# Kernel tuning notes

Hardware: AMD Instinct MI355X
Metric: run time of the kernel (lower is better)

The kernel has to match this reference:

```python
import jax, jax.numpy as jnp
import numpy as np

N_NODES = 100_000
N_EDGES = 600_000
D = 128  # in_channels


def setup_inputs() -> dict:
    key = jax.random.key(0)
    k1, k2, k3, k4, k5 = jax.random.split(key, 5)
    node_embs_src = jax.random.normal(k1, (N_NODES, D), dtype=jnp.float32)
    node_embs_dst = jax.random.normal(k2, (N_NODES, D), dtype=jnp.float32)
    edge_index = jax.random.randint(k3, (2, N_EDGES), 0, N_NODES, dtype=jnp.int64)
    # MLP params: Linear(2D -> D), Linear(D -> 1); scaled like default torch init
    W1 = jax.random.normal(k4, (2 * D, D), dtype=jnp.float32) / np.sqrt(2 * D)
    b1 = jnp.zeros((D,), dtype=jnp.float32)
    W2 = jax.random.normal(k5, (D, 1), dtype=jnp.float32) / np.sqrt(D)
    b2 = jnp.zeros((1,), dtype=jnp.float32)
    return {
        "node_embs_src": node_embs_src,
        "node_embs_dst": node_embs_dst,
        "edge_index": edge_index,
        "W1": W1,
        "b1": b1,
        "W2": W2,
        "b2": b2,
    }


def reference(node_embs_src, node_embs_dst, edge_index, W1, b1, W2, b2):
    # Gather per-edge source / destination embeddings: [E, D] each
    src = node_embs_src[edge_index[0]]
    dst = node_embs_dst[edge_index[1]]
    # concat([src, dst]) @ W1 == src @ W1[:D] + dst @ W1[D:]  (avoids materializing [E, 2D])
    h = jnp.dot(src, W1[:D]) + jnp.dot(dst, W1[D:]) + b1  # [E, D]
    h = jax.nn.relu(h)
    logits = jnp.dot(h, W2) + b2  # [E, 1]
    return jax.nn.sigmoid(logits)
```

## Files before the change

### kernel.cpp

```cpp
#include <hip/hip_runtime.h>
#include <stdint.h>

typedef __attribute__((ext_vector_type(8))) short short8;
typedef __attribute__((ext_vector_type(8))) signed char schar8;
typedef __attribute__((ext_vector_type(4))) float f32x4;

__device__ __forceinline__ unsigned short f2bf(float f) {
  union { float f; uint32_t u; } v; v.f = f;
  uint32_t u = v.u;
  uint32_t r = (u + 0x7FFFu + ((u >> 16) & 1u)) >> 16;
  return (unsigned short)r;
}
__device__ __forceinline__ float bf2f(unsigned short h) {
  union { uint32_t u; float f; } v; v.u = ((uint32_t)h) << 16; return v.f;
}

#define NBM 64
__global__ __launch_bounds__(256, 4)
void node_phase_q8(const float* __restrict__ src_emb,
                   const float* __restrict__ dst_emb,
                   const float* __restrict__ W1,
                   const float* __restrict__ b1,
                   int8_t* __restrict__ Q,
                   float* __restrict__ SC,
                   int Nn, int ntiles) {
  __shared__ __align__(16) char Als[NBM * 256];
  __shared__ __align__(16) float pam[NBM][4];

  const int tbl = blockIdx.y;
  const float* emb = tbl ? dst_emb : src_emb;
  const float* Wt  = W1 + (size_t)tbl * 128 * 128;
  int8_t* Qt  = Q  + (size_t)tbl * Nn * 128;
  float*  SCt = SC + (size_t)tbl * Nn;

  const int tid  = threadIdx.x;
  const int lane = tid & 63;
  const int w    = tid >> 6;
  const int l15  = lane & 15;
  const int lk8  = (lane >> 4) * 8;

  short8 bfrag[4][2];
#pragma unroll
  for (int s = 0; s < 4; ++s) {
#pragma unroll
    for (int nf = 0; nf < 2; ++nf) {
      const int col = w * 32 + 2 * l15 + nf;
      short8 t;
#pragma unroll
      for (int j = 0; j < 8; ++j) {
        const int k = s * 32 + lk8 + j;
        t[j] = (short)f2bf(Wt[k * 128 + col]);
      }
      bfrag[s][nf] = t;
    }
  }
  const int colb = w * 32 + 2 * l15;
  const float bias0 = tbl ? 0.f : b1[colb];
  const float bias1 = tbl ? 0.f : b1[colb + 1];

  const int q = tid & 15, r0 = tid >> 4;
  const int swz = (l15 & 7) << 4;
  const int gx = gridDim.x;

  float4 p0[4], p1[4];
#pragma unroll
  for (int i = 0; i < 4; ++i) {
    const int node = blockIdx.x * NBM + i * 16 + r0;
    if (node < Nn) {
      const float* base = emb + (size_t)node * 128 + q * 8;
      p0[i] = *(const float4*)base;
      p1[i] = *(const float4*)(base + 4);
    }
  }

  for (int t = blockIdx.x; t < ntiles; t += gx) {
    const int t0 = t * NBM;

#pragma unroll
    for (int i = 0; i < 4; ++i) {
      const int row = i * 16 + r0;
      short8 hv;
      hv[0] = (short)f2bf(p0[i].x); hv[1] = (short)f2bf(p0[i].y);
      hv[2] = (short)f2bf(p0[i].z); hv[3] = (short)f2bf(p0[i].w);
      hv[4] = (short)f2bf(p1[i].x); hv[5] = (short)f2bf(p1[i].y);
      hv[6] = (short)f2bf(p1[i].z); hv[7] = (short)f2bf(p1[i].w);
      const int byteoff = row * 256 + ((q * 16) ^ ((row & 7) << 4));
      *(short8*)(Als + byteoff) = hv;
    }
    __syncthreads();

    const int tn = t + gx;
    if (tn < ntiles) {
#pragma unroll
      for (int i = 0; i < 4; ++i) {
        const int node = tn * NBM + i * 16 + r0;
        if (node < Nn) {
          const float* base = emb + (size_t)node * 128 + q * 8;
          p0[i] = *(const float4*)base;
          p1[i] = *(const float4*)(base + 4);
        }
      }
    }

    f32x4 h0[4], h1[4];
#pragma unroll
    for (int m = 0; m < 4; ++m) {
      f32x4 acc0 = {0.f, 0.f, 0.f, 0.f};
      f32x4 acc1 = {0.f, 0.f, 0.f, 0.f};
      const int rowb = (m * 16 + l15) * 256;
      const int kb0  = lk8 * 2;
#pragma unroll
      for (int s = 0; s < 4; ++s) {
        const int off = rowb + ((s * 64 + kb0) ^ swz);
        const short8 a = *(const short8*)(Als + off);
        acc0 = __builtin_amdgcn_mfma_f32_16x16x32_bf16(a, bfrag[s][0], acc0, 0, 0, 0);
        acc1 = __builtin_amdgcn_mfma_f32_16x16x32_bf16(a, bfrag[s][1], acc1, 0, 0, 0);
      }
#pragma unroll
      for (int reg = 0; reg < 4; ++reg) {
        h0[m][reg] = acc0[reg] + bias0;
        h1[m][reg] = acc1[reg] + bias1;
        float pm = fmaxf(fabsf(h0[m][reg]), fabsf(h1[m][reg]));
        pm = fmaxf(pm, __shfl_xor(pm, 1, 16));
        pm = fmaxf(pm, __shfl_xor(pm, 2, 16));
        pm = fmaxf(pm, __shfl_xor(pm, 4, 16));
        pm = fmaxf(pm, __shfl_xor(pm, 8, 16));
        if (l15 == 0) pam[m * 16 + (lane >> 4) * 4 + reg][w] = pm;
      }
    }
    __syncthreads();

#pragma unroll
    for (int m = 0; m < 4; ++m) {
#pragma unroll
      for (int reg = 0; reg < 4; ++reg) {
        const int row  = m * 16 + (lane >> 4) * 4 + reg;
        const int node = t0 + row;
        const f32x4 pa = *(const f32x4*)pam[row];
        float am = fmaxf(fmaxf(pa[0], pa[1]), fmaxf(pa[2], pa[3]));
        am = fmaxf(am, 1e-20f);
        const float rq = 127.0f / am;
        if (node < Nn) {
          const int q0 = (int)rintf(h0[m][reg] * rq);
          const int q1 = (int)rintf(h1[m][reg] * rq);
          *(unsigned short*)(Qt + (size_t)node * 128 + colb) =
              (unsigned short)((q0 & 255) | ((q1 & 255) << 8));
          if ((tid & 15) == 0 && tid < 64)
            SCt[node] = am * (1.0f / 127.0f);
        }
      }
    }
    __syncthreads();
  }
}

__global__ __launch_bounds__(256, 8)
void edge_phase_q8(const int8_t* __restrict__ Qu,
                   const int8_t* __restrict__ Qv,
                   const float* __restrict__ scu,
                   const float* __restrict__ scv,
                   const int* __restrict__ eidx,
                   const float* __restrict__ W2,
                   const float* __restrict__ b2,
                   float* __restrict__ out,
                   int E) {
  const int tid = threadIdx.x;
  const int l15 = tid & 15;
  const int sg  = tid >> 4;

  float w2s[8];
#pragma unroll
  for (int j = 0; j < 8; ++j) w2s[j] = W2[l15 * 8 + j];
  const float b2s = b2[0];
  const int stride = gridDim.x * 16;

#pragma unroll 2
  for (int e = blockIdx.x * 16 + sg; e < E; e += stride) {
    const int s = eidx[e];
    const int d = eidx[E + e];
    const schar8 qu = *(const schar8*)(Qu + (size_t)s * 128 + l15 * 8);
    const schar8 qv = *(const schar8*)(Qv + (size_t)d * 128 + l15 * 8);
    const float su = scu[s];
    const float sv = scv[d];
    float acc = 0.f;
#pragma unroll
    for (int j = 0; j < 8; ++j) {
      float g = (float)(int)qu[j] * su + (float)(int)qv[j] * sv;
      g = g > 0.f ? g : 0.f;
      acc = fmaf(g, w2s[j], acc);
    }
    acc += __shfl_xor(acc, 1, 16);
    acc += __shfl_xor(acc, 2, 16);
    acc += __shfl_xor(acc, 4, 16);
    acc += __shfl_xor(acc, 8, 16);
    if (l15 == 0) out[e] = 1.f / (1.f + __expf(-(acc + b2s)));
  }
}

#define BM 64
__global__ __launch_bounds__(256, 4)
void edge_decoder_fused(const float* __restrict__ src_emb,
                        const float* __restrict__ dst_emb,
                        const int* __restrict__ eidx,
                        const float* __restrict__ W1,
                        const float* __restrict__ b1,
                        const float* __restrict__ W2,
                        const float* __restrict__ b2,
                        float* __restrict__ out,
                        int E, int ntiles) {
  __shared__ __align__(16) char Als[BM * 512];
  __shared__ float rowpart[4][BM];

  const int tid  = threadIdx.x;
  const int lane = tid & 63;
  const int w    = tid >> 6;
  const int l15  = lane & 15;
  const int lk8  = (lane >> 4) * 8;

  short8 bfrag[8][2];
#pragma unroll
  for (int s = 0; s < 8; ++s) {
#pragma unroll
    for (int nf = 0; nf < 2; ++nf) {
      const int col = w * 32 + nf * 16 + l15;
      short8 t;
#pragma unroll
      for (int j = 0; j < 8; ++j) {
        const int k = s * 32 + lk8 + j;
        t[j] = (short)f2bf(W1[k * 128 + col]);
      }
      bfrag[s][nf] = t;
    }
  }
  float b1v[2], w2v[2];
#pragma unroll
  for (int nf = 0; nf < 2; ++nf) {
    const int col = w * 32 + nf * 16 + l15;
    b1v[nf] = b1[col];
    w2v[nf] = W2[col];
  }
  const float b2s = b2[0];

  const int q  = tid & 31;
  const int r0 = tid >> 5;
  const int qq = q & 15;
  const bool is_src = (q < 16);
  const int swz = (l15 & 7) << 4;

  for (int t = blockIdx.x; t < ntiles; t += gridDim.x) {
    const int t0 = t * BM;
#pragma unroll
    for (int i = 0; i < 8; ++i) {
      const int row = i * 8 + r0;
      const int e = t0 + row;
      if (e < E) {
        const int node = is_src ? eidx[e] : eidx[E + e];
        const float* base = (is_src ? src_emb : dst_emb) + (size_t)node * 128 + qq * 8;
        const float4 f0 = *(const float4*)base;
        const float4 f1 = *(const float4*)(base + 4);
        short8 hv;
        hv[0] = (short)f2bf(f0.x); hv[1] = (short)f2bf(f0.y);
        hv[2] = (short)f2bf(f0.z); hv[3] = (short)f2bf(f0.w);
        hv[4] = (short)f2bf(f1.x); hv[5] = (short)f2bf(f1.y);
        hv[6] = (short)f2bf(f1.z); hv[7] = (short)f2bf(f1.w);
        const int byteoff = row * 512 + ((q * 16) ^ ((row & 7) << 4));
        *(short8*)(Als + byteoff) = hv;
      }
    }
    __syncthreads();

    for (int m = 0; m < 4; ++m) {
      f32x4 acc0 = {0.f, 0.f, 0.f, 0.f};
      f32x4 acc1 = {0.f, 0.f, 0.f, 0.f};
      const int rowb = (m * 16 + l15) * 512;
      const int kb0  = lk8 * 2;
#pragma unroll
      for (int s = 0; s < 8; ++s) {
        const int off = rowb + ((s * 64 + kb0) ^ swz);
        const short8 a = *(const short8*)(Als + off);
        acc0 = __builtin_amdgcn_mfma_f32_16x16x32_bf16(a, bfrag[s][0], acc0, 0, 0, 0);
        acc1 = __builtin_amdgcn_mfma_f32_16x16x32_bf16(a, bfrag[s][1], acc1, 0, 0, 0);
      }
      float pr[4];
#pragma unroll
      for (int reg = 0; reg < 4; ++reg) {
        float h0 = acc0[reg] + b1v[0]; h0 = h0 > 0.f ? h0 : 0.f;
        float h1 = acc1[reg] + b1v[1]; h1 = h1 > 0.f ? h1 : 0.f;
        pr[reg] = h0 * w2v[0] + h1 * w2v[1];
      }
#pragma unroll
      for (int off = 1; off < 16; off <<= 1) {
#pragma unroll
        for (int reg = 0; reg < 4; ++reg)
          pr[reg] += __shfl_xor(pr[reg], off, 64);
      }
      if (l15 == 0) {
        const int rbase = m * 16 + (lane >> 4) * 4;
#pragma unroll
        for (int reg = 0; reg < 4; ++reg)
          rowpart[w][rbase + reg] = pr[reg];
      }
    }
    __syncthreads();

    if (tid < BM) {
      const int e = t0 + tid;
      if (e < E) {
        const float sum = rowpart[0][tid] + rowpart[1][tid] +
                          rowpart[2][tid] + rowpart[3][tid] + b2s;
        out[e] = 1.f / (1.f + __expf(-sum));
      }
    }
    __syncthreads();
  }
}

extern "C" void kernel_launch(void* const* d_in, const int* in_sizes, int n_in,
                              void* d_out, int out_size, void* d_ws, size_t ws_size,
                              hipStream_t stream) {
  const float* src = (const float*)d_in[0];
  const float* dst = (const float*)d_in[1];
  const int*   eix = (const int*)d_in[2];
  const float* W1  = (const float*)d_in[3];
  const float* b1  = (const float*)d_in[4];
  const float* W2  = (const float*)d_in[5];
  const float* b2  = (const float*)d_in[6];
  float* out = (float*)d_out;

  const int E  = in_sizes[2] / 2;
  const int Nn = in_sizes[0] / 128;
  const size_t q_bytes  = (size_t)2 * Nn * 128;
  const size_t sc_bytes = (size_t)2 * Nn * sizeof(float);

  if (ws_size >= q_bytes + sc_bytes) {
    int8_t* Q  = (int8_t*)d_ws;
    float*  SC = (float*)((char*)d_ws + q_bytes);
    const int ntiles_n = (Nn + NBM - 1) / NBM;
    const int gx = ntiles_n < 512 ? ntiles_n : 512;
    node_phase_q8<<<dim3(gx, 2), 256, 0, stream>>>(src, dst, W1, b1, Q, SC, Nn, ntiles_n);
    const int nchunks = (E + 15) / 16;
    const int nblk = nchunks < 2048 ? nchunks : 2048;
    edge_phase_q8<<<nblk, 256, 0, stream>>>(Q, Q + (size_t)Nn * 128, SC, SC + Nn,
                                            eix, W2, b2, out, E);
  } else {
    const int ntiles = (E + BM - 1) / BM;
    const int grid = ntiles < 2048 ? ntiles : 2048;
    edge_decoder_fused<<<grid, 256, 0, stream>>>(src, dst, eix, W1, b1, W2, b2,
                                                 out, E, ntiles);
  }
}
```

Baseline: 74.15 us.

## Stage W1 in LDS and give each wave full rows in node phase

The node-phase kernel now converts W1 to bf16 once per block and stores it in a swizzled LDS buffer. Previously each wave kept a 32-column slice of B fragments in registers. Each wave now computes all 128 output columns for its own 16 rows, so the per-row absmax for int8 quantization becomes a 16-lane shuffle reduction. This removes the shared pam array and one __syncthreads per tile, and each lane writes 8 packed bytes instead of 2. In exchange the kernel reads B fragments from LDS on every MFMA, uses 32KB more LDS, and lowers the occupancy target and grid size to 3 blocks and 384 tiles.

```diff
diff --git a/kernel.cpp b/kernel.cpp
--- a/kernel.cpp
+++ b/kernel.cpp
@@ -16,7 +16,7 @@
 }
 
 #define NBM 64
-__global__ __launch_bounds__(256, 4)
+__global__ __launch_bounds__(256, 3)
 void node_phase_q8(const float* __restrict__ src_emb,
                    const float* __restrict__ dst_emb,
                    const float* __restrict__ W1,
@@ -25,7 +25,7 @@
                    float* __restrict__ SC,
                    int Nn, int ntiles) {
   __shared__ __align__(16) char Als[NBM * 256];
-  __shared__ __align__(16) float pam[NBM][4];
+  __shared__ __align__(16) char Wlds[128 * 256];
 
   const int tbl = blockIdx.y;
   const float* emb = tbl ? dst_emb : src_emb;
@@ -37,29 +37,25 @@
   const int lane = tid & 63;
   const int w    = tid >> 6;
   const int l15  = lane & 15;
-  const int lk8  = (lane >> 4) * 8;
-
-  short8 bfrag[4][2];
-#pragma unroll
-  for (int s = 0; s < 4; ++s) {
-#pragma unroll
-    for (int nf = 0; nf < 2; ++nf) {
-      const int col = w * 32 + 2 * l15 + nf;
-      short8 t;
-#pragma unroll
-      for (int j = 0; j < 8; ++j) {
-        const int k = s * 32 + lk8 + j;
-        t[j] = (short)f2bf(Wt[k * 128 + col]);
-      }
-      bfrag[s][nf] = t;
-    }
-  }
-  const int colb = w * 32 + 2 * l15;
-  const float bias0 = tbl ? 0.f : b1[colb];
-  const float bias1 = tbl ? 0.f : b1[colb + 1];
+  const int lg   = lane >> 4;
+
+  for (int c = tid; c < 2048; c += 256) {
+    const int col = c >> 4;
+    const int k8  = (c & 15) * 8;
+    short8 t;
+#pragma unroll
+    for (int j = 0; j < 8; ++j)
+      t[j] = (short)f2bf(Wt[(size_t)(k8 + j) * 128 + col]);
+    const int byteoff = (col * 256 + k8 * 2) ^ (((col >> 3) & 7) << 4);
+    *(short8*)(Wlds + byteoff) = t;
+  }
+
+  float b1s[8];
+#pragma unroll
+  for (int j = 0; j < 8; ++j) b1s[j] = tbl ? 0.f : b1[l15 * 8 + j];
 
   const int q = tid & 15, r0 = tid >> 4;
-  const int swz = (l15 & 7) << 4;
+  const int swzA = (l15 & 7) << 4;
   const int gx = gridDim.x;
 
   float4 p0[4], p1[4];
@@ -102,52 +98,49 @@
       }
     }
 
-    f32x4 h0[4], h1[4];
-#pragma unroll
-    for (int m = 0; m < 4; ++m) {
-      f32x4 acc0 = {0.f, 0.f, 0.f, 0.f};
-      f32x4 acc1 = {0.f, 0.f, 0.f, 0.f};
-      const int rowb = (m * 16 + l15) * 256;
-      const int kb0  = lk8 * 2;
-#pragma unroll
-      for (int s = 0; s < 4; ++s) {
-        const int off = rowb + ((s * 64 + kb0) ^ swz);
-        const short8 a = *(const short8*)(Als + off);
-        acc0 = __builtin_amdgcn_mfma_f32_16x16x32_bf16(a, bfrag[s][0], acc0, 0, 0, 0);
-        acc1 = __builtin_amdgcn_mfma_f32_16x16x32_bf16(a, bfrag[s][1], acc1, 0, 0, 0);
-      }
-#pragma unroll
-      for (int reg = 0; reg < 4; ++reg) {
-        h0[m][reg] = acc0[reg] + bias0;
-        h1[m][reg] = acc1[reg] + bias1;
-        float pm = fmaxf(fabsf(h0[m][reg]), fabsf(h1[m][reg]));
-        pm = fmaxf(pm, __shfl_xor(pm, 1, 16));
-        pm = fmaxf(pm, __shfl_xor(pm, 2, 16));
-        pm = fmaxf(pm, __shfl_xor(pm, 4, 16));
-        pm = fmaxf(pm, __shfl_xor(pm, 8, 16));
-        if (l15 == 0) pam[m * 16 + (lane >> 4) * 4 + reg][w] = pm;
-      }
-    }
-    __syncthreads();
-
-#pragma unroll
-    for (int m = 0; m < 4; ++m) {
-#pragma unroll
-      for (int reg = 0; reg < 4; ++reg) {
-        const int row  = m * 16 + (lane >> 4) * 4 + reg;
-        const int node = t0 + row;
-        const f32x4 pa = *(const f32x4*)pam[row];
-        float am = fmaxf(fmaxf(pa[0], pa[1]), fmaxf(pa[2], pa[3]));
-        am = fmaxf(am, 1e-20f);
+    f32x4 acc[8];
+#pragma unroll
+    for (int cf = 0; cf < 8; ++cf) acc[cf] = (f32x4){0.f, 0.f, 0.f, 0.f};
+
+#pragma unroll
+    for (int s = 0; s < 4; ++s) {
+      const int aoff = (w * 16 + l15) * 256 + ((s * 64 + lg * 16) ^ swzA);
+      const short8 a = *(const short8*)(Als + aoff);
+#pragma unroll
+      for (int cf = 0; cf < 8; ++cf) {
+        const int col = l15 * 8 + cf;
+        const int boff = (col * 256 + s * 64 + lg * 16) ^ (((col >> 3) & 7) << 4);
+        const short8 b = *(const short8*)(Wlds + boff);
+        acc[cf] = __builtin_amdgcn_mfma_f32_16x16x32_bf16(a, b, acc[cf], 0, 0, 0);
+      }
+    }
+
+#pragma unroll
+    for (int reg = 0; reg < 4; ++reg) {
+      float h[8];
+      float am = 1e-20f;
+#pragma unroll
+      for (int cf = 0; cf < 8; ++cf) {
+        h[cf] = acc[cf][reg] + b1s[cf];
+        am = fmaxf(am, fabsf(h[cf]));
+      }
+      am = fmaxf(am, __shfl_xor(am, 1, 16));
+      am = fmaxf(am, __shfl_xor(am, 2, 16));
+      am = fmaxf(am, __shfl_xor(am, 4, 16));
+      am = fmaxf(am, __shfl_xor(am, 8, 16));
+      const int node = t0 + w * 16 + lg * 4 + reg;
+      if (node < Nn) {
         const float rq = 127.0f / am;
-        if (node < Nn) {
-          const int q0 = (int)rintf(h0[m][reg] * rq);
-          const int q1 = (int)rintf(h1[m][reg] * rq);
-          *(unsigned short*)(Qt + (size_t)node * 128 + colb) =
-              (unsigned short)((q0 & 255) | ((q1 & 255) << 8));
-          if ((tid & 15) == 0 && tid < 64)
-            SCt[node] = am * (1.0f / 127.0f);
-        }
+        uint32_t lo = 0, hi = 0;
+#pragma unroll
+        for (int cf = 0; cf < 4; ++cf)
+          lo |= ((uint32_t)((int)rintf(h[cf] * rq) & 255)) << (8 * cf);
+#pragma unroll
+        for (int cf = 4; cf < 8; ++cf)
+          hi |= ((uint32_t)((int)rintf(h[cf] * rq) & 255)) << (8 * (cf - 4));
+        uint2 pk; pk.x = lo; pk.y = hi;
+        *(uint2*)(Qt + (size_t)node * 128 + l15 * 8) = pk;
+        if (l15 == 0) SCt[node] = am * (1.0f / 127.0f);
       }
     }
     __syncthreads();
@@ -336,7 +329,7 @@
     int8_t* Q  = (int8_t*)d_ws;
     float*  SC = (float*)((char*)d_ws + q_bytes);
     const int ntiles_n = (Nn + NBM - 1) / NBM;
-    const int gx = ntiles_n < 512 ? ntiles_n : 512;
+    const int gx = ntiles_n < 384 ? ntiles_n : 384;
     node_phase_q8<<<dim3(gx, 2), 256, 0, stream>>>(src, dst, W1, b1, Q, SC, Nn, ntiles_n);
     const int nchunks = (E + 15) / 16;
     const int nblk = nchunks < 2048 ? nchunks : 2048;
```

Result: no change. 75.62 us (+2.0%).

## Split node-phase quantization into separate bf16 store and row-quantize kernels

Applied to the files above, without the earlier changes.

The node-phase kernel now writes bf16 projections to workspace without the cross-wave absmax reduction and extra barrier. A new kernel then reads those rows back, computes per-row absmax and int8-quantizes them for the existing int8 edge kernel. A bf16 edge-kernel fallback is added for smaller workspaces. This removes LDS reductions and a sync from the MFMA kernel, at the cost of an extra kernel launch and an additional round-trip of about 51MB of bf16 data through memory.

```diff
diff --git a/kernel.cpp b/kernel.cpp
--- a/kernel.cpp
+++ b/kernel.cpp
@@ -17,21 +17,18 @@
 
 #define NBM 64
 __global__ __launch_bounds__(256, 4)
-void node_phase_q8(const float* __restrict__ src_emb,
-                   const float* __restrict__ dst_emb,
-                   const float* __restrict__ W1,
-                   const float* __restrict__ b1,
-                   int8_t* __restrict__ Q,
-                   float* __restrict__ SC,
-                   int Nn, int ntiles) {
+void node_phase_bf16(const float* __restrict__ src_emb,
+                     const float* __restrict__ dst_emb,
+                     const float* __restrict__ W1,
+                     const float* __restrict__ b1,
+                     unsigned short* __restrict__ UV,
+                     int Nn, int ntiles) {
   __shared__ __align__(16) char Als[NBM * 256];
-  __shared__ __align__(16) float pam[NBM][4];
 
   const int tbl = blockIdx.y;
   const float* emb = tbl ? dst_emb : src_emb;
   const float* Wt  = W1 + (size_t)tbl * 128 * 128;
-  int8_t* Qt  = Q  + (size_t)tbl * Nn * 128;
-  float*  SCt = SC + (size_t)tbl * Nn;
+  unsigned short* outp = UV + (size_t)tbl * Nn * 128;
 
   const int tid  = threadIdx.x;
   const int lane = tid & 63;
@@ -102,7 +99,6 @@
       }
     }
 
-    f32x4 h0[4], h1[4];
 #pragma unroll
     for (int m = 0; m < 4; ++m) {
       f32x4 acc0 = {0.f, 0.f, 0.f, 0.f};
@@ -118,39 +114,51 @@
       }
 #pragma unroll
       for (int reg = 0; reg < 4; ++reg) {
-        h0[m][reg] = acc0[reg] + bias0;
-        h1[m][reg] = acc1[reg] + bias1;
-        float pm = fmaxf(fabsf(h0[m][reg]), fabsf(h1[m][reg]));
-        pm = fmaxf(pm, __shfl_xor(pm, 1, 16));
-        pm = fmaxf(pm, __shfl_xor(pm, 2, 16));
-        pm = fmaxf(pm, __shfl_xor(pm, 4, 16));
-        pm = fmaxf(pm, __shfl_xor(pm, 8, 16));
-        if (l15 == 0) pam[m * 16 + (lane >> 4) * 4 + reg][w] = pm;
+        const int orow = t0 + m * 16 + ((lane >> 4) * 4) + reg;
+        if (orow < Nn) {
+          const uint32_t pk = (uint32_t)f2bf(acc0[reg] + bias0) |
+                              ((uint32_t)f2bf(acc1[reg] + bias1) << 16);
+          *(uint32_t*)&outp[(size_t)orow * 128 + colb] = pk;
+        }
       }
     }
     __syncthreads();
-
-#pragma unroll
-    for (int m = 0; m < 4; ++m) {
-#pragma unroll
-      for (int reg = 0; reg < 4; ++reg) {
-        const int row  = m * 16 + (lane >> 4) * 4 + reg;
-        const int node = t0 + row;
-        const f32x4 pa = *(const f32x4*)pam[row];
-        float am = fmaxf(fmaxf(pa[0], pa[1]), fmaxf(pa[2], pa[3]));
-        am = fmaxf(am, 1e-20f);
-        const float rq = 127.0f / am;
-        if (node < Nn) {
-          const int q0 = (int)rintf(h0[m][reg] * rq);
-          const int q1 = (int)rintf(h1[m][reg] * rq);
-          *(unsigned short*)(Qt + (size_t)node * 128 + colb) =
-              (unsigned short)((q0 & 255) | ((q1 & 255) << 8));
-          if ((tid & 15) == 0 && tid < 64)
-            SCt[node] = am * (1.0f / 127.0f);
-        }
-      }
-    }
-    __syncthreads();
+  }
+}
+
+__global__ __launch_bounds__(256, 8)
+void quant_rows_q8(const unsigned short* __restrict__ UV,
+                   int8_t* __restrict__ Q,
+                   float* __restrict__ SC,
+                   int nrows) {
+  const int tid = threadIdx.x;
+  const int l15 = tid & 15;
+  const int stride = gridDim.x * 16;
+
+  for (int r = blockIdx.x * 16 + (tid >> 4); r < nrows; r += stride) {
+    const short8 v = *(const short8*)(UV + (size_t)r * 128 + l15 * 8);
+    float f[8];
+    float am = 1e-20f;
+#pragma unroll
+    for (int j = 0; j < 8; ++j) {
+      f[j] = bf2f((unsigned short)v[j]);
+      am = fmaxf(am, fabsf(f[j]));
+    }
+    am = fmaxf(am, __shfl_xor(am, 1, 16));
+    am = fmaxf(am, __shfl_xor(am, 2, 16));
+    am = fmaxf(am, __shfl_xor(am, 4, 16));
+    am = fmaxf(am, __shfl_xor(am, 8, 16));
+    const float rq = 127.0f / am;
+    uint32_t lo = 0, hi = 0;
+#pragma unroll
+    for (int j = 0; j < 4; ++j)
+      lo |= ((uint32_t)((int)rintf(f[j] * rq) & 255)) << (8 * j);
+#pragma unroll
+    for (int j = 4; j < 8; ++j)
+      hi |= ((uint32_t)((int)rintf(f[j] * rq) & 255)) << (8 * (j - 4));
+    uint2 pk; pk.x = lo; pk.y = hi;
+    *(uint2*)(Q + (size_t)r * 128 + l15 * 8) = pk;
+    if (l15 == 0) SC[r] = am * (1.0f / 127.0f);
   }
 }
 
@@ -186,6 +194,46 @@
 #pragma unroll
     for (int j = 0; j < 8; ++j) {
       float g = (float)(int)qu[j] * su + (float)(int)qv[j] * sv;
+      g = g > 0.f ? g : 0.f;
+      acc = fmaf(g, w2s[j], acc);
+    }
+    acc += __shfl_xor(acc, 1, 16);
+    acc += __shfl_xor(acc, 2, 16);
+    acc += __shfl_xor(acc, 4, 16);
+    acc += __shfl_xor(acc, 8, 16);
+    if (l15 == 0) out[e] = 1.f / (1.f + __expf(-(acc + b2s)));
+  }
+}
+
+__global__ __launch_bounds__(256, 8)
+void edge_phase_bf16(const unsigned short* __restrict__ UV,
+                     const int* __restrict__ eidx,
+                     const float* __restrict__ W2,
+                     const float* __restrict__ b2,
+                     float* __restrict__ out,
+                     int E, int Nn) {
+  const int tid = threadIdx.x;
+  const int l15 = tid & 15;
+  const int sg  = tid >> 4;
+
+  float w2s[8];
+#pragma unroll
+  for (int j = 0; j < 8; ++j) w2s[j] = W2[l15 * 8 + j];
+  const float b2s = b2[0];
+  const unsigned short* U = UV;
+  const unsigned short* V = UV + (size_t)Nn * 128;
+  const int stride = gridDim.x * 16;
+
+#pragma unroll 2
+  for (int e = blockIdx.x * 16 + sg; e < E; e += stride) {
+    const int s = eidx[e];
+    const int d = eidx[E + e];
+    const short8 u8 = *(const short8*)(U + (size_t)s * 128 + l15 * 8);
+    const short8 v8 = *(const short8*)(V + (size_t)d * 128 + l15 * 8);
+    float acc = 0.f;
+#pragma unroll
+    for (int j = 0; j < 8; ++j) {
+      float g = bf2f((unsigned short)u8[j]) + bf2f((unsigned short)v8[j]);
       g = g > 0.f ? g : 0.f;
       acc = fmaf(g, w2s[j], acc);
     }
@@ -329,19 +377,29 @@
 
   const int E  = in_sizes[2] / 2;
   const int Nn = in_sizes[0] / 128;
-  const size_t q_bytes  = (size_t)2 * Nn * 128;
-  const size_t sc_bytes = (size_t)2 * Nn * sizeof(float);
-
-  if (ws_size >= q_bytes + sc_bytes) {
-    int8_t* Q  = (int8_t*)d_ws;
-    float*  SC = (float*)((char*)d_ws + q_bytes);
-    const int ntiles_n = (Nn + NBM - 1) / NBM;
-    const int gx = ntiles_n < 512 ? ntiles_n : 512;
-    node_phase_q8<<<dim3(gx, 2), 256, 0, stream>>>(src, dst, W1, b1, Q, SC, Nn, ntiles_n);
-    const int nchunks = (E + 15) / 16;
-    const int nblk = nchunks < 2048 ? nchunks : 2048;
+  const int nrows = 2 * Nn;
+  const size_t uv_bytes = (size_t)nrows * 128 * 2;
+  const size_t q_bytes  = (size_t)nrows * 128;
+  const size_t sc_bytes = (size_t)nrows * sizeof(float);
+
+  const int ntiles_n = (Nn + NBM - 1) / NBM;
+  const int gx = ntiles_n < 512 ? ntiles_n : 512;
+  const int nchunks = (E + 15) / 16;
+  const int nblk = nchunks < 2048 ? nchunks : 2048;
+
+  if (ws_size >= uv_bytes + q_bytes + sc_bytes) {
+    unsigned short* UV = (unsigned short*)d_ws;
+    int8_t* Q  = (int8_t*)((char*)d_ws + uv_bytes);
+    float*  SC = (float*)((char*)d_ws + uv_bytes + q_bytes);
+    node_phase_bf16<<<dim3(gx, 2), 256, 0, stream>>>(src, dst, W1, b1, UV, Nn, ntiles_n);
+    const int qblk = ((nrows + 15) / 16) < 2048 ? ((nrows + 15) / 16) : 2048;
+    quant_rows_q8<<<qblk, 256, 0, stream>>>(UV, Q, SC, nrows);
     edge_phase_q8<<<nblk, 256, 0, stream>>>(Q, Q + (size_t)Nn * 128, SC, SC + Nn,
                                             eix, W2, b2, out, E);
+  } else if (ws_size >= uv_bytes) {
+    unsigned short* UV = (unsigned short*)d_ws;
+    node_phase_bf16<<<dim3(gx, 2), 256, 0, stream>>>(src, dst, W1, b1, UV, Nn, ntiles_n);
+    edge_phase_bf16<<<nblk, 256, 0, stream>>>(UV, eix, W2, b2, out, E, Nn);
   } else {
     const int ntiles = (E + BM - 1) / BM;
     const int grid = ntiles < 2048 ? ntiles : 2048;
```

Measured after the change: 74.23 us. Within noise of the previous version (+0.1%).
